# Kernel optimization log

Measured on AMD Instinct MI355X. Metric: run time of the kernel, lower is better.

## Reference

```python
import jax, jax.numpy as jnp
import numpy as np

N, C, H, W = 4, 256, 64, 64  # in_channels == out_channels == C


def conv1x1(x, w, b):
    # x: [N, Cin, H, W], w: [Cout, Cin], b: [Cout]
    return jnp.einsum('nchw,oc->nohw', x, w) + b[None, :, None, None]


def setup_inputs() -> dict:
    key = jax.random.key(0)
    ks = jax.random.split(key, 4)
    scale = 1.0 / np.sqrt(C)
    return {
        'x': jax.random.normal(ks[0], (N, C, H, W), dtype=jnp.float32),
        'theta_w': jax.random.normal(ks[1], (C, C), dtype=jnp.float32) * scale,
        'theta_b': jnp.zeros((C,), dtype=jnp.float32),
        'phi_w': jax.random.normal(ks[2], (C, C), dtype=jnp.float32) * scale,
        'phi_b': jnp.zeros((C,), dtype=jnp.float32),
        'conv1_w': jax.random.normal(ks[3], (C, C), dtype=jnp.float32) * scale,
        'conv1_b': jnp.zeros((C,), dtype=jnp.float32),
    }


def reference(x, theta_w, theta_b, phi_w, phi_b, conv1_w, conv1_b):
    n, c, h, w = x.shape
    hw = h * w
    theta = conv1x1(x, theta_w, theta_b).reshape(n, c, hw)   # queries [N,C,HW]
    phi = conv1x1(x, phi_w, phi_b).reshape(n, c, hw)         # keys    [N,C,HW]
    g = x.reshape(n, c, hw)                                   # values  [N,C,HW]
    # f = einsum('niab,nicd->nabcd') flattened: [N, HW_q, HW_k]
    scores = jnp.einsum('ncp,ncq->npq', theta, phi) / jnp.sqrt(jnp.asarray(c, x.dtype))
    attn = jax.nn.softmax(scores, axis=-1)                    # softmax over keys
    # f = einsum('nabcd,nicd->niab'): weighted sum of values
    f = jnp.einsum('npq,ncq->ncp', attn, g).reshape(n, c, h, w)
    result = conv1x1(f, conv1_w, conv1_b)
    return x + result
```

## Files before the change

kernel.cpp:

```cpp
#include <hip/hip_runtime.h>
#include <hip/hip_bf16.h>

typedef __attribute__((ext_vector_type(8))) short short8;
typedef __attribute__((ext_vector_type(4))) short short4_t;
typedef __attribute__((ext_vector_type(4))) float float4_t;
typedef unsigned short ushort;

#define HW 4096
#define CC 256
#define NBATCH 4
#define SEQ ((size_t)NBATCH * HW)

static __device__ __forceinline__ unsigned short f2b(float f) {
    union { float f; unsigned u; } v; v.f = f;
    unsigned r = v.u + 0x7FFF + ((v.u >> 16) & 1);
    return (unsigned short)(r >> 16);
}
static __device__ __forceinline__ float b2f(unsigned short u) {
    union { unsigned u; float f; } v; v.u = ((unsigned)u) << 16;
    return v.f;
}
static __device__ __forceinline__ unsigned pk2(float a, float b) {
    __hip_bfloat162 h = __float22bfloat162_rn(make_float2(a, b));
    union { __hip_bfloat162 h; unsigned u; } v; v.h = h; return v.u;
}

__global__ __launch_bounds__(256) void k_prep(const float* __restrict__ x,
                                              const float* __restrict__ tw,
                                              const float* __restrict__ pw,
                                              const float* __restrict__ cw,
                                              unsigned short* __restrict__ XT,
                                              unsigned short* __restrict__ gb,
                                              unsigned short* __restrict__ Wbt,
                                              unsigned short* __restrict__ Wbp,
                                              unsigned short* __restrict__ Wbc) {
    __shared__ float T[64][65];
    int fb = blockIdx.x + 64 * (blockIdx.y + 4 * blockIdx.z);
    if (fb < 768) {
        int i = fb * 256 + threadIdx.x;
        int sel = i >> 16, off = i & 65535;
        const float* s = sel == 0 ? tw : (sel == 1 ? pw : cw);
        unsigned short* d = sel == 0 ? Wbt : (sel == 1 ? Wbp : Wbc);
        d[off] = f2b(s[off]);
    }
    int n = blockIdx.z, c0 = blockIdx.y * 64, p0 = blockIdx.x * 64;
    int t = threadIdx.x;
    int pl = t & 63, rg = t >> 6;
    const float* xp = x + ((size_t)n * CC + c0) * HW + p0;
    #pragma unroll
    for (int i = 0; i < 16; i++) {
        int cl = rg * 16 + i;
        float v = xp[(size_t)cl * HW + pl];
        T[cl][pl] = v;
        gb[((size_t)n * CC + c0 + cl) * HW + p0 + pl] = f2b(v);
    }
    __syncthreads();
    int cl = t & 63, pg = t >> 6;
    unsigned short* xt = XT + ((size_t)n * HW + p0) * CC + c0;
    #pragma unroll
    for (int i = 0; i < 16; i++) {
        int plw = pg * 16 + i;
        xt[(size_t)plw * CC + cl] = f2b(T[cl][plw]);
    }
}

__global__ __launch_bounds__(256) void k_proj(const unsigned short* __restrict__ XT,
                                              const unsigned short* __restrict__ Wt,
                                              const unsigned short* __restrict__ Wp,
                                              const float* __restrict__ bt,
                                              const float* __restrict__ bp,
                                              unsigned short* __restrict__ outT_t,
                                              unsigned short* __restrict__ outT_p) {
    const unsigned short* W; const float* b; unsigned short* outT;
    if (blockIdx.y == 0) { W = Wt; b = bt; outT = outT_t; }
    else                 { W = Wp; b = bp; outT = outT_p; }
    int w = threadIdx.x >> 6, lane = threadIdx.x & 63;
    int nidx = lane & 15, quad = lane >> 4;
    size_t row0 = (size_t)blockIdx.x * 64 + w * 16;
    float4_t acc[16];
    #pragma unroll
    for (int i = 0; i < 16; i++) acc[i] = (float4_t)(0.f);
    const unsigned short* arow = XT + (row0 + nidx) * CC + quad * 8;
    for (int ks = 0; ks < 8; ks++) {
        short8 a = *(const short8*)(arow + ks * 32);
        #pragma unroll
        for (int cb = 0; cb < 16; cb++) {
            short8 bb = *(const short8*)(W + (size_t)(cb * 16 + nidx) * CC + ks * 32 + quad * 8);
            acc[cb] = __builtin_amdgcn_mfma_f32_16x16x32_bf16(a, bb, acc[cb], 0, 0, 0);
        }
    }
    #pragma unroll
    for (int cb = 0; cb < 16; cb++) {
        int co = cb * 16 + nidx;
        float bias = b[co];
        #pragma unroll
        for (int r = 0; r < 4; r++) {
            size_t prow = row0 + quad * 4 + r;
            outT[prow * CC + co] = f2b(acc[cb][r] + bias);
        }
    }
}

__global__ __launch_bounds__(512)
void k_attn(const unsigned short* __restrict__ thetaT,
            const unsigned short* __restrict__ phiT,
            const unsigned short* __restrict__ gb,
            ushort* __restrict__ Ow, float* __restrict__ lw) {
    __shared__ __align__(16) ushort Kl[2][16384];
    __shared__ __align__(16) ushort Pbuf[2][16][64][8];
    __shared__ float Lbuf[2][128];

    const int tid = threadIdx.x;
    const int w = tid >> 6, lane = tid & 63;
    const int nidx = lane & 15, quad = lane >> 4;
    const int qg = w & 3;
    const int kh = w >> 2;
    const int nb = (blockIdx.x & 7) >> 1;
    const int h  = blockIdx.x & 1;
    const int qtile = blockIdx.x >> 3;
    const int p0 = qtile * 128;
    const size_t seq0 = (size_t)nb * HW;
    const ushort* Kg = phiT + seq0 * CC;
    const ushort* Vg = gb + (size_t)nb * CC * HW;
    const int k00 = h * 2048;

    short8 th[2][8];
    #pragma unroll
    for (int qs = 0; qs < 2; qs++) {
        const ushort* qrow = thetaT + (seq0 + p0 + qg * 32 + qs * 16 + nidx) * CC + quad * 8;
        #pragma unroll
        for (int kb = 0; kb < 8; kb++) th[qs][kb] = *(const short8*)(qrow + kb * 32);
    }

    float4_t o[2][8];
    #pragma unroll
    for (int i = 0; i < 2; i++)
        #pragma unroll
        for (int j = 0; j < 8; j++) o[i][j] = (float4_t)(0.f);
    float lrow[2] = {0.f, 0.f};

    const int c_s = tid >> 4, n_s = tid & 15;
    const int kfbase = (c_s >> 2) * 512 + ((c_s & 3) * 16 + n_s) * 8;
    auto loadKregs = [&](short8 (&kr)[4], int tt) {
        #pragma unroll
        for (int rr = 0; rr < 4; rr++)
            kr[rr] = *(const short8*)(Kg + (size_t)(k00 + tt * 64 + rr * 16 + n_s) * CC + c_s * 8);
    };
    auto stageK = [&](int buf, const short8 (&kr)[4]) {
        #pragma unroll
        for (int rr = 0; rr < 4; rr++) *(short8*)(&Kl[buf][rr * 4096 + kfbase]) = kr[rr];
    };
    auto loadVregs = [&](short8 (&vr)[4], int tt) {
        #pragma unroll
        for (int mg = 0; mg < 2; mg++)
            #pragma unroll
            for (int kst = 0; kst < 2; kst++)
                vr[mg * 2 + kst] = *(const short8*)(Vg + (size_t)(w * 32 + mg * 16 + nidx) * HW
                                                    + k00 + tt * 64 + kst * 32 + quad * 8);
    };

    const float SC = 0.0625f * 1.44269504088896f;
    const int Gp = quad >> 1;
    const int pcell_lo = (nidx ^ (Gp * 4));
    const int pj0 = (quad & 1) * 4;
    const int prcell = ((lane >> 4) << 4) | ((lane & 15) ^ (((lane >> 4) & 1) * 4));

    float4_t s00, s01, s10, s11;
    auto expPhase = [&](int buf) {
        {
            float e0 = exp2f(s00[0] * SC), e1 = exp2f(s00[1] * SC);
            float e2 = exp2f(s00[2] * SC), e3 = exp2f(s00[3] * SC);
            lrow[0] += (e0 + e1) + (e2 + e3);
            uint2 pk; pk.x = pk2(e0, e1); pk.y = pk2(e2, e3);
            *(uint2*)(&Pbuf[buf][(qg * 2 + 0) * 2 + kh][(0 * 2 + Gp) * 16 + pcell_lo][pj0]) = pk;
        }
        {
            float e0 = exp2f(s01[0] * SC), e1 = exp2f(s01[1] * SC);
            float e2 = exp2f(s01[2] * SC), e3 = exp2f(s01[3] * SC);
            lrow[1] += (e0 + e1) + (e2 + e3);
            uint2 pk; pk.x = pk2(e0, e1); pk.y = pk2(e2, e3);
            *(uint2*)(&Pbuf[buf][(qg * 2 + 1) * 2 + kh][(0 * 2 + Gp) * 16 + pcell_lo][pj0]) = pk;
        }
        {
            float e0 = exp2f(s10[0] * SC), e1 = exp2f(s10[1] * SC);
            float e2 = exp2f(s10[2] * SC), e3 = exp2f(s10[3] * SC);
            lrow[0] += (e0 + e1) + (e2 + e3);
            uint2 pk; pk.x = pk2(e0, e1); pk.y = pk2(e2, e3);
            *(uint2*)(&Pbuf[buf][(qg * 2 + 0) * 2 + kh][(1 * 2 + Gp) * 16 + pcell_lo][pj0]) = pk;
        }
        {
            float e0 = exp2f(s11[0] * SC), e1 = exp2f(s11[1] * SC);
            float e2 = exp2f(s11[2] * SC), e3 = exp2f(s11[3] * SC);
            lrow[1] += (e0 + e1) + (e2 + e3);
            uint2 pk; pk.x = pk2(e0, e1); pk.y = pk2(e2, e3);
            *(uint2*)(&Pbuf[buf][(qg * 2 + 1) * 2 + kh][(1 * 2 + Gp) * 16 + pcell_lo][pj0]) = pk;
        }
    };

    short8 kregs[4], vA[4], vB[4];

    auto ITER = [&](int t, const short8 (&vCur)[4], short8 (&vNext)[4]) {
        const int pb = t & 1;
        const int kbuf = (t + 1) & 1;
        s00 = (float4_t)(0.f); s01 = (float4_t)(0.f);
        s10 = (float4_t)(0.f); s11 = (float4_t)(0.f);
        #pragma unroll
        for (int i = 0; i < 8; i++) {
            short8 k0 = *(const short8*)(&Kl[kbuf][((kh * 2 + 0) * 8 + i) * 512 + lane * 8]);
            short8 k1 = *(const short8*)(&Kl[kbuf][((kh * 2 + 1) * 8 + i) * 512 + lane * 8]);
            s00 = __builtin_amdgcn_mfma_f32_16x16x32_bf16(k0, th[0][i], s00, 0, 0, 0);
            s01 = __builtin_amdgcn_mfma_f32_16x16x32_bf16(k0, th[1][i], s01, 0, 0, 0);
            s10 = __builtin_amdgcn_mfma_f32_16x16x32_bf16(k1, th[0][i], s10, 0, 0, 0);
            s11 = __builtin_amdgcn_mfma_f32_16x16x32_bf16(k1, th[1][i], s11, 0, 0, 0);
            short8 pf0 = *(const short8*)(&Pbuf[pb][i * 2 + 0][prcell][0]);
            short8 pf1 = *(const short8*)(&Pbuf[pb][i * 2 + 1][prcell][0]);
            o[0][i] = __builtin_amdgcn_mfma_f32_16x16x32_bf16(vCur[0], pf0, o[0][i], 0, 0, 0);
            o[0][i] = __builtin_amdgcn_mfma_f32_16x16x32_bf16(vCur[1], pf1, o[0][i], 0, 0, 0);
            o[1][i] = __builtin_amdgcn_mfma_f32_16x16x32_bf16(vCur[2], pf0, o[1][i], 0, 0, 0);
            o[1][i] = __builtin_amdgcn_mfma_f32_16x16x32_bf16(vCur[3], pf1, o[1][i], 0, 0, 0);
        }
        loadVregs(vNext, t + 1);
        expPhase((t + 1) & 1);
        if (t < 30) {
            stageK((t + 2) & 1, kregs);
            loadKregs(kregs, (t + 3 < 32) ? t + 3 : 31);
        }
        __syncthreads();
    };

    loadKregs(kregs, 0); loadVregs(vA, 0);
    stageK(0, kregs);
    loadKregs(kregs, 1);
    __syncthreads();
    s00 = (float4_t)(0.f); s01 = (float4_t)(0.f); s10 = (float4_t)(0.f); s11 = (float4_t)(0.f);
    #pragma unroll
    for (int kb = 0; kb < 8; kb++) {
        short8 k0 = *(const short8*)(&Kl[0][((kh * 2 + 0) * 8 + kb) * 512 + lane * 8]);
        short8 k1 = *(const short8*)(&Kl[0][((kh * 2 + 1) * 8 + kb) * 512 + lane * 8]);
        s00 = __builtin_amdgcn_mfma_f32_16x16x32_bf16(k0, th[0][kb], s00, 0, 0, 0);
        s01 = __builtin_amdgcn_mfma_f32_16x16x32_bf16(k0, th[1][kb], s01, 0, 0, 0);
        s10 = __builtin_amdgcn_mfma_f32_16x16x32_bf16(k1, th[0][kb], s10, 0, 0, 0);
        s11 = __builtin_amdgcn_mfma_f32_16x16x32_bf16(k1, th[1][kb], s11, 0, 0, 0);
    }
    expPhase(0);
    stageK(1, kregs);
    loadKregs(kregs, 2);
    __syncthreads();

    #pragma unroll 1
    for (int tt = 0; tt < 15; tt++) {
        ITER(tt * 2, vA, vB);
        ITER(tt * 2 + 1, vB, vA);
    }
    ITER(30, vA, vB);
    #pragma unroll
    for (int i = 0; i < 8; i++) {
        short8 pf0 = *(const short8*)(&Pbuf[1][i * 2 + 0][prcell][0]);
        short8 pf1 = *(const short8*)(&Pbuf[1][i * 2 + 1][prcell][0]);
        o[0][i] = __builtin_amdgcn_mfma_f32_16x16x32_bf16(vB[0], pf0, o[0][i], 0, 0, 0);
        o[0][i] = __builtin_amdgcn_mfma_f32_16x16x32_bf16(vB[1], pf1, o[0][i], 0, 0, 0);
        o[1][i] = __builtin_amdgcn_mfma_f32_16x16x32_bf16(vB[2], pf0, o[1][i], 0, 0, 0);
        o[1][i] = __builtin_amdgcn_mfma_f32_16x16x32_bf16(vB[3], pf1, o[1][i], 0, 0, 0);
    }

    #pragma unroll
    for (int qs = 0; qs < 2; qs++) {
        float v = lrow[qs];
        v += __shfl_xor(v, 16);
        v += __shfl_xor(v, 32);
        if (quad == 0) Lbuf[kh][qg * 32 + qs * 16 + nidx] = v;
    }
    __syncthreads();
    if (tid < 128)
        lw[(size_t)h * SEQ + seq0 + p0 + tid] = Lbuf[0][tid] + Lbuf[1][tid];
    ushort* Op = Ow + ((size_t)h * SEQ + seq0 + p0) * CC;
    #pragma unroll
    for (int mg = 0; mg < 2; mg++)
        #pragma unroll
        for (int qq = 0; qq < 8; qq++) {
            uint2 pk;
            pk.x = pk2(o[mg][qq][0], o[mg][qq][1]);
            pk.y = pk2(o[mg][qq][2], o[mg][qq][3]);
            *(uint2*)(Op + (size_t)(qq * 16 + nidx) * CC + w * 32 + mg * 16 + quad * 4) = pk;
        }
}

__global__ __launch_bounds__(256) void k_reduce(const ushort* __restrict__ Ow,
                                                const float* __restrict__ lw,
                                                unsigned short* __restrict__ fT) {
    const short8* O0 = (const short8*)Ow;
    const short8* O1 = (const short8*)(Ow + SEQ * CC);
    int i0 = blockIdx.x * 256 + threadIdx.x;
    #pragma unroll
    for (int j = 0; j < 4; j++) {
        int idx = j * 131072 + i0;
        int row = idx >> 5;
        float li = 1.0f / (lw[row] + lw[SEQ + row]);
        short8 a = O0[idx];
        short8 b = O1[idx];
        short8 pk;
        #pragma unroll
        for (int r = 0; r < 8; r++)
            pk[r] = (short)f2b((b2f((ushort)a[r]) + b2f((ushort)b[r])) * li);
        *(short8*)(fT + (size_t)idx * 8) = pk;
    }
}

__global__ __launch_bounds__(256) void k_final(const unsigned short* __restrict__ Wc,
                                               const float* __restrict__ bc,
                                               const unsigned short* __restrict__ fT,
                                               const float* __restrict__ x,
                                               float* __restrict__ out) {
    int w = threadIdx.x >> 6, lane = threadIdx.x & 63;
    int nidx = lane & 15, quad = lane >> 4;
    int n = blockIdx.z;
    int co0 = blockIdx.y * 64 + w * 16;
    int p0 = blockIdx.x * 64;
    float4_t acc[4];
    #pragma unroll
    for (int i = 0; i < 4; i++) acc[i] = (float4_t)(0.f);
    const unsigned short* arow = Wc + (size_t)(co0 + nidx) * CC + quad * 8;
    const unsigned short* brow = fT + ((size_t)n * HW + p0 + nidx) * CC + quad * 8;
    for (int ks = 0; ks < 8; ks++) {
        short8 a = *(const short8*)(arow + ks * 32);
        #pragma unroll
        for (int pb = 0; pb < 4; pb++) {
            short8 bb = *(const short8*)(brow + (size_t)pb * 16 * CC + ks * 32);
            acc[pb] = __builtin_amdgcn_mfma_f32_16x16x32_bf16(a, bb, acc[pb], 0, 0, 0);
        }
    }
    #pragma unroll
    for (int pb = 0; pb < 4; pb++) {
        #pragma unroll
        for (int r = 0; r < 4; r++) {
            int co = co0 + quad * 4 + r;
            size_t idx = ((size_t)n * CC + co) * HW + p0 + pb * 16 + nidx;
            out[idx] = x[idx] + bc[co] + acc[pb][r];
        }
    }
}

extern "C" void kernel_launch(void* const* d_in, const int* in_sizes, int n_in,
                              void* d_out, int out_size, void* d_ws, size_t ws_size,
                              hipStream_t stream) {
    const float* x       = (const float*)d_in[0];
    const float* theta_w = (const float*)d_in[1];
    const float* theta_b = (const float*)d_in[2];
    const float* phi_w   = (const float*)d_in[3];
    const float* phi_b   = (const float*)d_in[4];
    const float* conv1_w = (const float*)d_in[5];
    const float* conv1_b = (const float*)d_in[6];
    float* out = (float*)d_out;

    unsigned short* XT  = (unsigned short*)d_ws;
    unsigned short* gb  = XT  + SEQ * CC;
    unsigned short* thT = gb  + SEQ * CC;
    unsigned short* phT = thT + SEQ * CC;
    unsigned short* fT  = phT + SEQ * CC;
    unsigned short* Wbt = fT  + SEQ * CC;
    unsigned short* Wbp = Wbt + 65536;
    unsigned short* Wbc = Wbp + 65536;
    unsigned short* Ow  = Wbc + 65536;
    float* lw = (float*)(Ow + 2 * SEQ * CC);

    k_prep<<<dim3(64, 4, 4), 256, 0, stream>>>(x, theta_w, phi_w, conv1_w, XT, gb, Wbt, Wbp, Wbc);
    k_proj<<<dim3(256, 2), 256, 0, stream>>>(XT, Wbt, Wbp, theta_b, phi_b, thT, phT);
    k_attn<<<dim3(256), 512, 0, stream>>>(thT, phT, gb, Ow, lw);
    k_reduce<<<dim3(512), 256, 0, stream>>>(Ow, lw, fT);
    k_final<<<dim3(64, 4, 4), 256, 0, stream>>>(Wbc, conv1_b, fT, x, out);
}
```

Baseline: 212.7 us.

## Fuse split-KV reduction into final conv and tune attention barriers/priority

The separate k_reduce kernel is removed. k_final now reads both partial attention outputs and the row sums, normalises them into a swizzled LDS tile, and runs the output 1x1 conv from LDS with 512 threads covering all 256 output channels per block. This cuts one launch and the fT round trip through global memory. In the attention kernel, __syncthreads is replaced with an LDS-only waitcnt plus s_barrier and a sched_barrier, and wave priority is raised around the MFMA loop. The final kernel now has a smaller grid (256 blocks), which may lower its parallelism.

```diff
diff --git a/kernel.cpp b/kernel.cpp
--- a/kernel.cpp
+++ b/kernel.cpp
@@ -23,6 +23,12 @@
 static __device__ __forceinline__ unsigned pk2(float a, float b) {
     __hip_bfloat162 h = __float22bfloat162_rn(make_float2(a, b));
     union { __hip_bfloat162 h; unsigned u; } v; v.h = h; return v.u;
+}
+
+static __device__ __forceinline__ void barrier_lds() {
+    asm volatile("s_waitcnt lgkmcnt(0)" ::: "memory");
+    __builtin_amdgcn_s_barrier();
+    __builtin_amdgcn_sched_barrier(0);
 }
 
 __global__ __launch_bounds__(256) void k_prep(const float* __restrict__ x,
@@ -204,6 +210,7 @@
         const int kbuf = (t + 1) & 1;
         s00 = (float4_t)(0.f); s01 = (float4_t)(0.f);
         s10 = (float4_t)(0.f); s11 = (float4_t)(0.f);
+        __builtin_amdgcn_s_setprio(1);
         #pragma unroll
         for (int i = 0; i < 8; i++) {
             short8 k0 = *(const short8*)(&Kl[kbuf][((kh * 2 + 0) * 8 + i) * 512 + lane * 8]);
@@ -219,20 +226,22 @@
             o[1][i] = __builtin_amdgcn_mfma_f32_16x16x32_bf16(vCur[2], pf0, o[1][i], 0, 0, 0);
             o[1][i] = __builtin_amdgcn_mfma_f32_16x16x32_bf16(vCur[3], pf1, o[1][i], 0, 0, 0);
         }
+        __builtin_amdgcn_s_setprio(0);
         loadVregs(vNext, t + 1);
         expPhase((t + 1) & 1);
         if (t < 30) {
             stageK((t + 2) & 1, kregs);
             loadKregs(kregs, (t + 3 < 32) ? t + 3 : 31);
         }
-        __syncthreads();
+        barrier_lds();
     };
 
     loadKregs(kregs, 0); loadVregs(vA, 0);
     stageK(0, kregs);
     loadKregs(kregs, 1);
-    __syncthreads();
+    barrier_lds();
     s00 = (float4_t)(0.f); s01 = (float4_t)(0.f); s10 = (float4_t)(0.f); s11 = (float4_t)(0.f);
+    __builtin_amdgcn_s_setprio(1);
     #pragma unroll
     for (int kb = 0; kb < 8; kb++) {
         short8 k0 = *(const short8*)(&Kl[0][((kh * 2 + 0) * 8 + kb) * 512 + lane * 8]);
@@ -242,10 +251,11 @@
         s10 = __builtin_amdgcn_mfma_f32_16x16x32_bf16(k1, th[0][kb], s10, 0, 0, 0);
         s11 = __builtin_amdgcn_mfma_f32_16x16x32_bf16(k1, th[1][kb], s11, 0, 0, 0);
     }
+    __builtin_amdgcn_s_setprio(0);
     expPhase(0);
     stageK(1, kregs);
     loadKregs(kregs, 2);
-    __syncthreads();
+    barrier_lds();
 
     #pragma unroll 1
     for (int tt = 0; tt < 15; tt++) {
@@ -285,57 +295,77 @@
         }
 }
 
-__global__ __launch_bounds__(256) void k_reduce(const ushort* __restrict__ Ow,
-                                                const float* __restrict__ lw,
-                                                unsigned short* __restrict__ fT) {
-    const short8* O0 = (const short8*)Ow;
-    const short8* O1 = (const short8*)(Ow + SEQ * CC);
-    int i0 = blockIdx.x * 256 + threadIdx.x;
-    #pragma unroll
-    for (int j = 0; j < 4; j++) {
-        int idx = j * 131072 + i0;
-        int row = idx >> 5;
-        float li = 1.0f / (lw[row] + lw[SEQ + row]);
-        short8 a = O0[idx];
-        short8 b = O1[idx];
-        short8 pk;
-        #pragma unroll
-        for (int r = 0; r < 8; r++)
-            pk[r] = (short)f2b((b2f((ushort)a[r]) + b2f((ushort)b[r])) * li);
-        *(short8*)(fT + (size_t)idx * 8) = pk;
-    }
-}
-
-__global__ __launch_bounds__(256) void k_final(const unsigned short* __restrict__ Wc,
-                                               const float* __restrict__ bc,
-                                               const unsigned short* __restrict__ fT,
-                                               const float* __restrict__ x,
-                                               float* __restrict__ out) {
-    int w = threadIdx.x >> 6, lane = threadIdx.x & 63;
-    int nidx = lane & 15, quad = lane >> 4;
-    int n = blockIdx.z;
-    int co0 = blockIdx.y * 64 + w * 16;
-    int p0 = blockIdx.x * 64;
-    float4_t acc[4];
-    #pragma unroll
-    for (int i = 0; i < 4; i++) acc[i] = (float4_t)(0.f);
-    const unsigned short* arow = Wc + (size_t)(co0 + nidx) * CC + quad * 8;
-    const unsigned short* brow = fT + ((size_t)n * HW + p0 + nidx) * CC + quad * 8;
+__global__ __launch_bounds__(512)
+void k_final(const unsigned short* __restrict__ Wc,
+             const float* __restrict__ bc,
+             const ushort* __restrict__ Ow,
+             const float* __restrict__ lw,
+             const float* __restrict__ x,
+             float* __restrict__ out) {
+    __shared__ __align__(16) ushort F[64][256];
+    const int n = blockIdx.z;
+    const int p0 = blockIdx.x * 64;
+    const int tid = threadIdx.x;
+
+    {
+        const int r = tid >> 3;
+        const int c0 = tid & 7;
+        const size_t grow = (size_t)n * HW + p0 + r;
+        const float li = 1.0f / (lw[grow] + lw[SEQ + grow]);
+        const short8* O0 = (const short8*)(Ow + grow * CC);
+        const short8* O1 = (const short8*)(Ow + SEQ * CC + grow * CC);
+        #pragma unroll
+        for (int i = 0; i < 4; i++) {
+            int ch = c0 + 8 * i;
+            short8 a = O0[ch];
+            short8 b = O1[ch];
+            union { short8 s; unsigned u[4]; } pk;
+            float f[8];
+            #pragma unroll
+            for (int j = 0; j < 8; j++)
+                f[j] = (b2f((ushort)a[j]) + b2f((ushort)b[j])) * li;
+            pk.u[0] = pk2(f[0], f[1]); pk.u[1] = pk2(f[2], f[3]);
+            pk.u[2] = pk2(f[4], f[5]); pk.u[3] = pk2(f[6], f[7]);
+            int swz = ch ^ (r & 7);
+            *(short8*)(&F[r][swz * 8]) = pk.s;
+        }
+    }
+    __syncthreads();
+
+    const int w = tid >> 6, lane = tid & 63;
+    const int nidx = lane & 15, quad = lane >> 4;
+    const int co_base = w * 32;
+    float4_t acc[2][4];
+    #pragma unroll
+    for (int i = 0; i < 2; i++)
+        #pragma unroll
+        for (int j = 0; j < 4; j++) acc[i][j] = (float4_t)(0.f);
+
+    const unsigned short* a0row = Wc + (size_t)(co_base + nidx) * CC + quad * 8;
+    const unsigned short* a1row = Wc + (size_t)(co_base + 16 + nidx) * CC + quad * 8;
     for (int ks = 0; ks < 8; ks++) {
-        short8 a = *(const short8*)(arow + ks * 32);
+        short8 a0 = *(const short8*)(a0row + ks * 32);
+        short8 a1 = *(const short8*)(a1row + ks * 32);
         #pragma unroll
         for (int pb = 0; pb < 4; pb++) {
-            short8 bb = *(const short8*)(brow + (size_t)pb * 16 * CC + ks * 32);
-            acc[pb] = __builtin_amdgcn_mfma_f32_16x16x32_bf16(a, bb, acc[pb], 0, 0, 0);
-        }
-    }
-    #pragma unroll
-    for (int pb = 0; pb < 4; pb++) {
-        #pragma unroll
-        for (int r = 0; r < 4; r++) {
-            int co = co0 + quad * 4 + r;
-            size_t idx = ((size_t)n * CC + co) * HW + p0 + pb * 16 + nidx;
-            out[idx] = x[idx] + bc[co] + acc[pb][r];
+            int row = pb * 16 + nidx;
+            int chunk = (ks * 4 + quad) ^ (row & 7);
+            short8 bb = *(const short8*)(&F[row][chunk * 8]);
+            acc[0][pb] = __builtin_amdgcn_mfma_f32_16x16x32_bf16(a0, bb, acc[0][pb], 0, 0, 0);
+            acc[1][pb] = __builtin_amdgcn_mfma_f32_16x16x32_bf16(a1, bb, acc[1][pb], 0, 0, 0);
+        }
+    }
+
+    #pragma unroll
+    for (int cb = 0; cb < 2; cb++) {
+        #pragma unroll
+        for (int pb = 0; pb < 4; pb++) {
+            #pragma unroll
+            for (int r2 = 0; r2 < 4; r2++) {
+                int co = co_base + cb * 16 + quad * 4 + r2;
+                size_t idx = ((size_t)n * CC + co) * HW + p0 + pb * 16 + nidx;
+                out[idx] = x[idx] + bc[co] + acc[cb][pb][r2];
+            }
         }
     }
 }
@@ -366,6 +396,5 @@
     k_prep<<<dim3(64, 4, 4), 256, 0, stream>>>(x, theta_w, phi_w, conv1_w, XT, gb, Wbt, Wbp, Wbc);
     k_proj<<<dim3(256, 2), 256, 0, stream>>>(XT, Wbt, Wbp, theta_b, phi_b, thT, phT);
     k_attn<<<dim3(256), 512, 0, stream>>>(thT, phT, gb, Ow, lw);
-    k_reduce<<<dim3(512), 256, 0, stream>>>(Ow, lw, fT);
-    k_final<<<dim3(64, 4, 4), 256, 0, stream>>>(Wbc, conv1_b, fT, x, out);
-}
+    k_final<<<dim3(64, 1, 4), 512, 0, stream>>>(Wbc, conv1_b, Ow, lw, x, out);
+}
```

New measurement: 203.4 us. 1.05x faster.
